# Kernel tuning notes

Measured on AMD Instinct MI355X. Metric: run time of the kernel, lower is better.

The kernel has to match this reference:

```python
import jax, jax.numpy as jnp
import numpy as np

N_NODES = 100000
N_EDGES = 3200000
F_IN = 512
HIDDEN = 64
N_CLASSES = 64


def setup_inputs() -> dict:
    key = jax.random.key(0)
    ks = jax.random.split(key, 6)
    node_features = jax.random.normal(ks[0], (N_NODES, F_IN), dtype=jnp.float32)
    edge_rows = jax.random.randint(ks[1], (N_EDGES,), 0, N_NODES, dtype=jnp.int32)
    edge_cols = jax.random.randint(ks[2], (N_EDGES,), 0, N_NODES, dtype=jnp.int32)
    edge_vals = jax.random.uniform(ks[3], (N_EDGES,), dtype=jnp.float32)
    W1 = jax.random.normal(ks[4], (F_IN, HIDDEN), dtype=jnp.float32) / np.sqrt(F_IN)
    b1 = jnp.zeros((HIDDEN,), dtype=jnp.float32)
    W2 = jax.random.normal(ks[5], (HIDDEN, N_CLASSES), dtype=jnp.float32) / np.sqrt(HIDDEN)
    b2 = jnp.zeros((N_CLASSES,), dtype=jnp.float32)
    return {
        "node_features": node_features,
        "edge_rows": edge_rows,
        "edge_cols": edge_cols,
        "edge_vals": edge_vals,
        "W1": W1,
        "b1": b1,
        "W2": W2,
        "b2": b2,
    }


def reference(node_features, edge_rows, edge_cols, edge_vals, W1, b1, W2, b2):
    # MLP node transform (inference: dropout is identity, no norms)
    h = jax.nn.relu(node_features @ W1 + b1)          # [N, HIDDEN]
    logits = h @ W2 + b2                              # [N, C]
    # smoother @ logits : sparse [N,N] COO times dense [N,C]
    messages = edge_vals[:, None] * logits[edge_cols]  # [E, C]
    out = jax.ops.segment_sum(messages, edge_rows, num_segments=N_NODES)
    return out
```

## Files before the change

kernel.cpp:

```cpp
#include <hip/hip_runtime.h>
#include <hip/hip_bf16.h>
#include <stdint.h>

#define N_NODES 100000
#define N_EDGES 3200000
#define F_IN    512
#define HIDDEN  64
#define NCLS    64

#define BROWS   128
#define NBKT    782
#define NBKT_PAD 1024
#define CHUNK   4096
#define EPB     16384
#define NCB     ((N_EDGES + EPB - 1) / EPB)

typedef float v4f __attribute__((ext_vector_type(4)));
typedef short v8s __attribute__((ext_vector_type(8)));

__device__ __forceinline__ unsigned short f2bf(float f){
  unsigned u = __float_as_uint(f);
  u += 0x7fffu + ((u >> 16) & 1u);
  return (unsigned short)(u >> 16);
}
__device__ __forceinline__ float bflo(unsigned u){ return __uint_as_float(u << 16); }
__device__ __forceinline__ float bfhi(unsigned u){ return __uint_as_float(u & 0xffff0000u); }

__global__ void prep_weights(const float* __restrict__ W1, const float* __restrict__ W2,
                             unsigned short* __restrict__ w1f, unsigned short* __restrict__ w2f){
  int t = blockIdx.x * 256 + threadIdx.x;
  if (t < 16*4*64*8){
    int j = t & 7, lane = (t >> 3) & 63, nt = (t >> 9) & 3, ks = t >> 11;
    int m = lane & 15, q = lane >> 4;
    int k = ks*32 + q*8 + j, n = nt*16 + m;
    w1f[t] = f2bf(W1[k*HIDDEN + n]);
  } else {
    int u = t - 16*4*64*8;
    if (u < 2*4*64*8){
      int j = u & 7, lane = (u >> 3) & 63, nt = (u >> 9) & 3, ks = u >> 11;
      int m = lane & 15, q = lane >> 4;
      int k = ks*32 + q*8 + j, n = nt*16 + m;
      w2f[u] = f2bf(W2[k*NCLS + n]);
    }
  }
}

__global__ __launch_bounds__(256) void mlp_kernel(
    const float* __restrict__ X, const float* __restrict__ b1,
    const float* __restrict__ b2,
    const unsigned short* __restrict__ w1f, const unsigned short* __restrict__ w2f,
    unsigned short* __restrict__ logits){
  __shared__ __align__(16) float lds[4][16][68];
  int tid  = threadIdx.x;
  int wid  = tid >> 6, lane = tid & 63;
  int m    = lane & 15, q = lane >> 4;
  int base = blockIdx.x * 64 + wid * 16;
  if (base > N_NODES - 16) base = N_NODES - 16;

  const float* rp = X + (size_t)(base + m) * F_IN + q * 8;
  const v8s* w1v = (const v8s*)w1f;
  const v8s* w2v = (const v8s*)w2f;

  v4f a0c = {0,0,0,0}, a1c = {0,0,0,0}, a2c = {0,0,0,0}, a3c = {0,0,0,0};
  #pragma unroll
  for (int ks = 0; ks < 16; ++ks){
    const float4* pa = (const float4*)(rp + ks * 32);
    float4 x0 = pa[0], x1 = pa[1];
    v8s af;
    af[0]=(short)f2bf(x0.x); af[1]=(short)f2bf(x0.y); af[2]=(short)f2bf(x0.z); af[3]=(short)f2bf(x0.w);
    af[4]=(short)f2bf(x1.x); af[5]=(short)f2bf(x1.y); af[6]=(short)f2bf(x1.z); af[7]=(short)f2bf(x1.w);
    a0c = __builtin_amdgcn_mfma_f32_16x16x32_bf16(af, w1v[(ks*4+0)*64 + lane], a0c, 0,0,0);
    a1c = __builtin_amdgcn_mfma_f32_16x16x32_bf16(af, w1v[(ks*4+1)*64 + lane], a1c, 0,0,0);
    a2c = __builtin_amdgcn_mfma_f32_16x16x32_bf16(af, w1v[(ks*4+2)*64 + lane], a2c, 0,0,0);
    a3c = __builtin_amdgcn_mfma_f32_16x16x32_bf16(af, w1v[(ks*4+3)*64 + lane], a3c, 0,0,0);
  }

  float b1v0 = b1[m], b1v1 = b1[16+m], b1v2 = b1[32+m], b1v3 = b1[48+m];
  #pragma unroll
  for (int r = 0; r < 4; ++r){
    int row = q*4 + r;
    lds[wid][row][     m] = fmaxf(a0c[r] + b1v0, 0.f);
    lds[wid][row][16 + m] = fmaxf(a1c[r] + b1v1, 0.f);
    lds[wid][row][32 + m] = fmaxf(a2c[r] + b1v2, 0.f);
    lds[wid][row][48 + m] = fmaxf(a3c[r] + b1v3, 0.f);
  }
  __syncthreads();

  v4f c0 = {0,0,0,0}, c1 = {0,0,0,0}, c2 = {0,0,0,0}, c3 = {0,0,0,0};
  #pragma unroll
  for (int k2 = 0; k2 < 2; ++k2){
    const float4* ph = (const float4*)&lds[wid][m][k2*32 + q*8];
    float4 h0 = ph[0], h1 = ph[1];
    v8s af;
    af[0]=(short)f2bf(h0.x); af[1]=(short)f2bf(h0.y); af[2]=(short)f2bf(h0.z); af[3]=(short)f2bf(h0.w);
    af[4]=(short)f2bf(h1.x); af[5]=(short)f2bf(h1.y); af[6]=(short)f2bf(h1.z); af[7]=(short)f2bf(h1.w);
    c0 = __builtin_amdgcn_mfma_f32_16x16x32_bf16(af, w2v[(k2*4+0)*64 + lane], c0, 0,0,0);
    c1 = __builtin_amdgcn_mfma_f32_16x16x32_bf16(af, w2v[(k2*4+1)*64 + lane], c1, 0,0,0);
    c2 = __builtin_amdgcn_mfma_f32_16x16x32_bf16(af, w2v[(k2*4+2)*64 + lane], c2, 0,0,0);
    c3 = __builtin_amdgcn_mfma_f32_16x16x32_bf16(af, w2v[(k2*4+3)*64 + lane], c3, 0,0,0);
  }

  float b2v0 = b2[m], b2v1 = b2[16+m], b2v2 = b2[32+m], b2v3 = b2[48+m];
  unsigned short* lp = logits + (size_t)base * NCLS;
  #pragma unroll
  for (int r = 0; r < 4; ++r){
    int row = q*4 + r;
    lp[row*NCLS +      m] = f2bf(c0[r] + b2v0);
    lp[row*NCLS + 16 + m] = f2bf(c1[r] + b2v1);
    lp[row*NCLS + 32 + m] = f2bf(c2[r] + b2v2);
    lp[row*NCLS + 48 + m] = f2bf(c3[r] + b2v3);
  }
}

__global__ __launch_bounds__(256) void bucket_count(
    const int* __restrict__ rows, int* __restrict__ bcnt){
  __shared__ int lc[NBKT_PAD];
  int t = threadIdx.x;
  #pragma unroll
  for (int i = 0; i < 4; ++i) lc[t*4 + i] = 0;
  __syncthreads();
  int base = blockIdx.x * EPB;
  int cnt  = min(EPB, N_EDGES - base);
  const int4* rp = (const int4*)(rows + base);
  int nv = cnt >> 2;
  for (int i = t; i < nv; i += 256){
    int4 r = rp[i];
    atomicAdd(&lc[r.x >> 7], 1);
    atomicAdd(&lc[r.y >> 7], 1);
    atomicAdd(&lc[r.z >> 7], 1);
    atomicAdd(&lc[r.w >> 7], 1);
  }
  __syncthreads();
  for (int i = t; i < NBKT; i += 256){
    int v = lc[i];
    if (v) atomicAdd(&bcnt[i], v);
  }
}

__global__ __launch_bounds__(256) void bucket_scan(
    const int* __restrict__ bcnt, int* __restrict__ bbase, int* __restrict__ bcur,
    int* __restrict__ offs){
  __shared__ int ssum[256];
  int t = threadIdx.x;
  int v[4]; int s = 0;
  #pragma unroll
  for (int k = 0; k < 4; ++k){
    int i = t*4 + k;
    v[k] = (i < NBKT) ? bcnt[i] : 0;
    s += v[k];
  }
  ssum[t] = s; __syncthreads();
  for (int o = 1; o < 256; o <<= 1){
    int add = (t >= o) ? ssum[t - o] : 0;
    __syncthreads();
    ssum[t] += add;
    __syncthreads();
  }
  int run = ssum[t] - s;
  #pragma unroll
  for (int k = 0; k < 4; ++k){
    int i = t*4 + k;
    if (i < NBKT){ bbase[i] = run; bcur[i] = run; run += v[k]; }
  }
  if (t == 0){ bbase[NBKT] = N_EDGES; offs[N_NODES] = N_EDGES; }
}

__global__ __launch_bounds__(256) void bucket_scatter(
    const int* __restrict__ rows, const int* __restrict__ cols,
    const float* __restrict__ vals, int* __restrict__ bcur,
    int2* __restrict__ ebkt){
  __shared__ int  lcnt[NBKT_PAD];
  __shared__ int  lbase[NBKT_PAD];
  __shared__ int  ssum[256];
  __shared__ int2 stage[CHUNK];
  __shared__ int  sdst[CHUNK];
  int t = threadIdx.x;
  int base = blockIdx.x * CHUNK;
  int cnt  = min(CHUNK, N_EDGES - base);

  #pragma unroll
  for (int i = 0; i < 4; ++i) lcnt[t*4 + i] = 0;
  __syncthreads();

  int r[16];
  #pragma unroll
  for (int k = 0; k < 16; ++k){
    int li = t + k*256;
    if (li < cnt){
      r[k] = rows[base + li];
      atomicAdd(&lcnt[r[k] >> 7], 1);
    } else r[k] = -1;
  }
  __syncthreads();

  int v0 = lcnt[t*4], v1 = lcnt[t*4+1], v2 = lcnt[t*4+2], v3 = lcnt[t*4+3];
  int s = v0 + v1 + v2 + v3;
  ssum[t] = s; __syncthreads();
  for (int o = 1; o < 256; o <<= 1){
    int add = (t >= o) ? ssum[t - o] : 0;
    __syncthreads();
    ssum[t] += add;
    __syncthreads();
  }
  int run = ssum[t] - s;
  int e0 = run, e1 = run + v0, e2 = run + v0 + v1, e3 = run + v0 + v1 + v2;
  if (v0){ int g = atomicAdd(&bcur[t*4+0], v0); lbase[t*4+0] = g - e0; }
  if (v1){ int g = atomicAdd(&bcur[t*4+1], v1); lbase[t*4+1] = g - e1; }
  if (v2){ int g = atomicAdd(&bcur[t*4+2], v2); lbase[t*4+2] = g - e2; }
  if (v3){ int g = atomicAdd(&bcur[t*4+3], v3); lbase[t*4+3] = g - e3; }
  lcnt[t*4+0] = e0; lcnt[t*4+1] = e1; lcnt[t*4+2] = e2; lcnt[t*4+3] = e3;
  __syncthreads();

  #pragma unroll
  for (int k = 0; k < 16; ++k){
    if (r[k] >= 0){
      int li = t + k*256;
      int c  = cols[base + li];
      float v = vals[base + li];
      int b  = r[k] >> 7;
      int pos = atomicAdd(&lcnt[b], 1);
      stage[pos] = make_int2(((r[k] & 127) << 17) | c, __float_as_int(v));
      sdst[pos]  = lbase[b];
    }
  }
  __syncthreads();

  for (int j = t; j < cnt; j += 256){
    ebkt[sdst[j] + j] = stage[j];
  }
}

__global__ __launch_bounds__(256) void bucket_sort(
    const int* __restrict__ bbase, const int2* __restrict__ ebkt,
    int2* __restrict__ edges, int* __restrict__ offs){
  __shared__ int rc[BROWS];
  __shared__ int sc[BROWS];
  __shared__ int cur[BROWS];
  int b = blockIdx.x, t = threadIdx.x;
  int row0 = b * BROWS;
  int s = bbase[b], e = bbase[b + 1];
  if (t < BROWS) rc[t] = 0;
  __syncthreads();
  for (int i = s + t; i < e; i += 256){
    int lr = ((unsigned)ebkt[i].x) >> 17;
    atomicAdd(&rc[lr], 1);
  }
  __syncthreads();
  if (t < BROWS) sc[t] = rc[t];
  __syncthreads();
  for (int o = 1; o < BROWS; o <<= 1){
    int add = (t >= o && t < BROWS) ? sc[t - o] : 0;
    __syncthreads();
    if (t < BROWS) sc[t] += add;
    __syncthreads();
  }
  if (t < BROWS){
    int off0 = s + sc[t] - rc[t];
    cur[t] = off0;
    int rr = row0 + t;
    if (rr < N_NODES) offs[rr] = off0;
  }
  __syncthreads();
  for (int i = s + t; i < e; i += 256){
    int2 ev = ebkt[i];
    int lr  = ((unsigned)ev.x) >> 17;
    int pos = atomicAdd(&cur[lr], 1);
    edges[pos] = make_int2(ev.x & 0x1FFFF, ev.y);
  }
}

__global__ __launch_bounds__(256) void agg_kernel(
    const int* __restrict__ offs, const int2* __restrict__ edges,
    const unsigned short* __restrict__ logits, float* __restrict__ out){
  int n    = blockIdx.x * 4 + (threadIdx.x >> 6);
  int lane = threadIdx.x & 63;
  int h    = lane & 15;
  int sel  = lane >> 4;
  int s = offs[n], e = offs[n + 1];
  const uint2* lg = (const uint2*)logits;

  float a0 = 0.f, a1 = 0.f, a2 = 0.f, a3 = 0.f;
  int i = s;
  for (; i + 16 <= e; i += 16){
    int2 e0 = edges[i      + sel];
    int2 e1 = edges[i + 4  + sel];
    int2 e2 = edges[i + 8  + sel];
    int2 e3 = edges[i + 12 + sel];
    uint2 u0 = lg[((size_t)e0.x << 4) + h];
    uint2 u1 = lg[((size_t)e1.x << 4) + h];
    uint2 u2 = lg[((size_t)e2.x << 4) + h];
    uint2 u3 = lg[((size_t)e3.x << 4) + h];
    float v0 = __int_as_float(e0.y), v1 = __int_as_float(e1.y);
    float v2 = __int_as_float(e2.y), v3 = __int_as_float(e3.y);
    a0 = fmaf(v0, bflo(u0.x), a0); a1 = fmaf(v0, bfhi(u0.x), a1);
    a2 = fmaf(v0, bflo(u0.y), a2); a3 = fmaf(v0, bfhi(u0.y), a3);
    a0 = fmaf(v1, bflo(u1.x), a0); a1 = fmaf(v1, bfhi(u1.x), a1);
    a2 = fmaf(v1, bflo(u1.y), a2); a3 = fmaf(v1, bfhi(u1.y), a3);
    a0 = fmaf(v2, bflo(u2.x), a0); a1 = fmaf(v2, bfhi(u2.x), a1);
    a2 = fmaf(v2, bflo(u2.y), a2); a3 = fmaf(v2, bfhi(u2.y), a3);
    a0 = fmaf(v3, bflo(u3.x), a0); a1 = fmaf(v3, bfhi(u3.x), a1);
    a2 = fmaf(v3, bflo(u3.y), a2); a3 = fmaf(v3, bfhi(u3.y), a3);
  }
  for (; i < e; i += 4){
    int idx = i + sel;
    int col = 0; float v = 0.f;
    if (idx < e){ int2 ev = edges[idx]; col = ev.x; v = __int_as_float(ev.y); }
    uint2 u = lg[((size_t)col << 4) + h];
    a0 = fmaf(v, bflo(u.x), a0); a1 = fmaf(v, bfhi(u.x), a1);
    a2 = fmaf(v, bflo(u.y), a2); a3 = fmaf(v, bfhi(u.y), a3);
  }
  a0 += __shfl_xor(a0, 16); a0 += __shfl_xor(a0, 32);
  a1 += __shfl_xor(a1, 16); a1 += __shfl_xor(a1, 32);
  a2 += __shfl_xor(a2, 16); a2 += __shfl_xor(a2, 32);
  a3 += __shfl_xor(a3, 16); a3 += __shfl_xor(a3, 32);
  if (sel == 0){
    float4* op = (float4*)(out + (size_t)n * NCLS);
    op[h] = make_float4(a0, a1, a2, a3);
  }
}

__global__ void scatter_atomic(const int* __restrict__ rows, const int* __restrict__ cols,
                               const float* __restrict__ vals,
                               const unsigned short* __restrict__ logits,
                               float* __restrict__ out){
  long g = (long)blockIdx.x * 256 + threadIdx.x;
  int e = (int)(g >> 6), c = (int)(g & 63);
  if (e < N_EDGES){
    float lv = __uint_as_float(((unsigned)logits[(size_t)cols[e] * NCLS + c]) << 16);
    atomicAdd(&out[(size_t)rows[e] * NCLS + c], vals[e] * lv);
  }
}

extern "C" void kernel_launch(void* const* d_in, const int* in_sizes, int n_in,
                              void* d_out, int out_size, void* d_ws, size_t ws_size,
                              hipStream_t stream){
  const float* X     = (const float*)d_in[0];
  const int*   erows = (const int*)  d_in[1];
  const int*   ecols = (const int*)  d_in[2];
  const float* evals = (const float*)d_in[3];
  const float* W1    = (const float*)d_in[4];
  const float* b1    = (const float*)d_in[5];
  const float* W2    = (const float*)d_in[6];
  const float* b2    = (const float*)d_in[7];
  float* out = (float*)d_out;

  char* ws = (char*)d_ws;
  size_t off = 0;
  auto alloc = [&](size_t bytes) -> char* {
    char* p = ws + off;
    off = (off + bytes + 255) & ~(size_t)255;
    return p;
  };
  unsigned short* logits = (unsigned short*)alloc((size_t)N_NODES * NCLS * 2);
  unsigned short* w1f    = (unsigned short*)alloc(16*4*64*8 * 2);
  unsigned short* w2f    = (unsigned short*)alloc(2*4*64*8 * 2);
  int* offs  = (int*)alloc((size_t)(N_NODES + 1) * 4);
  int* bcnt  = (int*)alloc((size_t)NBKT * 4);
  int* bbase = (int*)alloc((size_t)(NBKT + 1) * 4);
  int* bcur  = (int*)alloc((size_t)NBKT * 4);
  int2* ebkt  = (int2*)alloc((size_t)N_EDGES * 8);
  int2* edges = (int2*)alloc((size_t)N_EDGES * 8);
  size_t full_need = off;

  prep_weights<<<144, 256, 0, stream>>>(W1, W2, w1f, w2f);
  mlp_kernel<<<(N_NODES + 63) / 64, 256, 0, stream>>>(X, b1, b2, w1f, w2f, logits);

  if (ws_size >= full_need){
    hipMemsetAsync(bcnt, 0, (size_t)NBKT * 4, stream);
    bucket_count  <<<NCB, 256, 0, stream>>>(erows, bcnt);
    bucket_scan   <<<1, 256, 0, stream>>>(bcnt, bbase, bcur, offs);
    bucket_scatter<<<(N_EDGES + CHUNK - 1) / CHUNK, 256, 0, stream>>>(erows, ecols, evals, bcur, ebkt);
    bucket_sort   <<<NBKT, 256, 0, stream>>>(bbase, ebkt, edges, offs);
    agg_kernel    <<<N_NODES / 4, 256, 0, stream>>>(offs, edges, logits, out);
  } else {
    hipMemsetAsync(out, 0, (size_t)N_NODES * NCLS * 4, stream);
    scatter_atomic<<<(int)(((long)N_EDGES * 64 + 255) / 256), 256, 0, stream>>>(
        erows, ecols, evals, logits, out);
  }
}
```

Measured before the change: 519.4 us.

## Replace count/scan/sort pipeline with fixed-capacity buckets and LDS atomic aggregation

Drops the bucket count, scan and per-row sort kernels. Edges are now scattered into fixed-capacity per-bucket slots (CAP entries each), with a small overflow list, and a new per-bucket kernel accumulates 128 rows x 64 classes in shared memory using LDS atomics. Overflow edges are applied afterwards with global atomics, and counter zeroing is folded into the weight-prep kernel. This removes several launches and a full pass over the edge data, at the cost of heavy LDS atomic traffic and a capacity limit that leans on the roughly uniform row distribution.

```diff
diff --git a/kernel.cpp b/kernel.cpp
--- a/kernel.cpp
+++ b/kernel.cpp
@@ -12,8 +12,9 @@
 #define NBKT    782
 #define NBKT_PAD 1024
 #define CHUNK   4096
-#define EPB     16384
-#define NCB     ((N_EDGES + EPB - 1) / EPB)
+#define CAP     4608
+#define OVF_CAP 8192
+#define SENTINEL ((int)0x80000000)
 
 typedef float v4f __attribute__((ext_vector_type(4)));
 typedef short v8s __attribute__((ext_vector_type(8)));
@@ -24,11 +25,12 @@
   return (unsigned short)(u >> 16);
 }
 __device__ __forceinline__ float bflo(unsigned u){ return __uint_as_float(u << 16); }
-__device__ __forceinline__ float bfhi(unsigned u){ return __uint_as_float(u & 0xffff0000u); }
 
 __global__ void prep_weights(const float* __restrict__ W1, const float* __restrict__ W2,
-                             unsigned short* __restrict__ w1f, unsigned short* __restrict__ w2f){
+                             unsigned short* __restrict__ w1f, unsigned short* __restrict__ w2f,
+                             int* __restrict__ zeroc){
   int t = blockIdx.x * 256 + threadIdx.x;
+  if (t < NBKT*16 + 16) zeroc[t] = 0;
   if (t < 16*4*64*8){
     int j = t & 7, lane = (t >> 3) & 63, nt = (t >> 9) & 3, ks = t >> 11;
     int m = lane & 15, q = lane >> 4;
@@ -112,62 +114,10 @@
   }
 }
 
-__global__ __launch_bounds__(256) void bucket_count(
-    const int* __restrict__ rows, int* __restrict__ bcnt){
-  __shared__ int lc[NBKT_PAD];
-  int t = threadIdx.x;
-  #pragma unroll
-  for (int i = 0; i < 4; ++i) lc[t*4 + i] = 0;
-  __syncthreads();
-  int base = blockIdx.x * EPB;
-  int cnt  = min(EPB, N_EDGES - base);
-  const int4* rp = (const int4*)(rows + base);
-  int nv = cnt >> 2;
-  for (int i = t; i < nv; i += 256){
-    int4 r = rp[i];
-    atomicAdd(&lc[r.x >> 7], 1);
-    atomicAdd(&lc[r.y >> 7], 1);
-    atomicAdd(&lc[r.z >> 7], 1);
-    atomicAdd(&lc[r.w >> 7], 1);
-  }
-  __syncthreads();
-  for (int i = t; i < NBKT; i += 256){
-    int v = lc[i];
-    if (v) atomicAdd(&bcnt[i], v);
-  }
-}
-
-__global__ __launch_bounds__(256) void bucket_scan(
-    const int* __restrict__ bcnt, int* __restrict__ bbase, int* __restrict__ bcur,
-    int* __restrict__ offs){
-  __shared__ int ssum[256];
-  int t = threadIdx.x;
-  int v[4]; int s = 0;
-  #pragma unroll
-  for (int k = 0; k < 4; ++k){
-    int i = t*4 + k;
-    v[k] = (i < NBKT) ? bcnt[i] : 0;
-    s += v[k];
-  }
-  ssum[t] = s; __syncthreads();
-  for (int o = 1; o < 256; o <<= 1){
-    int add = (t >= o) ? ssum[t - o] : 0;
-    __syncthreads();
-    ssum[t] += add;
-    __syncthreads();
-  }
-  int run = ssum[t] - s;
-  #pragma unroll
-  for (int k = 0; k < 4; ++k){
-    int i = t*4 + k;
-    if (i < NBKT){ bbase[i] = run; bcur[i] = run; run += v[k]; }
-  }
-  if (t == 0){ bbase[NBKT] = N_EDGES; offs[N_NODES] = N_EDGES; }
-}
-
 __global__ __launch_bounds__(256) void bucket_scatter(
     const int* __restrict__ rows, const int* __restrict__ cols,
     const float* __restrict__ vals, int* __restrict__ bcur,
+    int* __restrict__ ovf_cnt, int4* __restrict__ ovf,
     int2* __restrict__ ebkt){
   __shared__ int  lcnt[NBKT_PAD];
   __shared__ int  lbase[NBKT_PAD];
@@ -204,10 +154,10 @@
   }
   int run = ssum[t] - s;
   int e0 = run, e1 = run + v0, e2 = run + v0 + v1, e3 = run + v0 + v1 + v2;
-  if (v0){ int g = atomicAdd(&bcur[t*4+0], v0); lbase[t*4+0] = g - e0; }
-  if (v1){ int g = atomicAdd(&bcur[t*4+1], v1); lbase[t*4+1] = g - e1; }
-  if (v2){ int g = atomicAdd(&bcur[t*4+2], v2); lbase[t*4+2] = g - e2; }
-  if (v3){ int g = atomicAdd(&bcur[t*4+3], v3); lbase[t*4+3] = g - e3; }
+  if (v0){ int g = atomicAdd(&bcur[(t*4+0)*16], v0); lbase[t*4+0] = (t*4+0)*CAP + g - e0; }
+  if (v1){ int g = atomicAdd(&bcur[(t*4+1)*16], v1); lbase[t*4+1] = (t*4+1)*CAP + g - e1; }
+  if (v2){ int g = atomicAdd(&bcur[(t*4+2)*16], v2); lbase[t*4+2] = (t*4+2)*CAP + g - e2; }
+  if (v3){ int g = atomicAdd(&bcur[(t*4+3)*16], v3); lbase[t*4+3] = (t*4+3)*CAP + g - e3; }
   lcnt[t*4+0] = e0; lcnt[t*4+1] = e1; lcnt[t*4+2] = e2; lcnt[t*4+3] = e3;
   __syncthreads();
 
@@ -219,103 +169,81 @@
       float v = vals[base + li];
       int b  = r[k] >> 7;
       int pos = atomicAdd(&lcnt[b], 1);
-      stage[pos] = make_int2(((r[k] & 127) << 17) | c, __float_as_int(v));
-      sdst[pos]  = lbase[b];
+      int dest = lbase[b] + pos;
+      if (dest < b*CAP + CAP){
+        stage[pos] = make_int2(((r[k] & 127) << 17) | c, __float_as_int(v));
+        sdst[pos]  = lbase[b];
+      } else {
+        sdst[pos] = SENTINEL;
+        int o = atomicAdd(ovf_cnt, 1);
+        if (o < OVF_CAP) ovf[o] = make_int4(r[k], c, __float_as_int(v), 0);
+      }
     }
   }
   __syncthreads();
 
   for (int j = t; j < cnt; j += 256){
-    ebkt[sdst[j] + j] = stage[j];
-  }
-}
-
-__global__ __launch_bounds__(256) void bucket_sort(
-    const int* __restrict__ bbase, const int2* __restrict__ ebkt,
-    int2* __restrict__ edges, int* __restrict__ offs){
-  __shared__ int rc[BROWS];
-  __shared__ int sc[BROWS];
-  __shared__ int cur[BROWS];
+    int d = sdst[j];
+    if (d != SENTINEL) ebkt[d + j] = stage[j];
+  }
+}
+
+__global__ __launch_bounds__(256) void bucket_agg(
+    const int* __restrict__ bcur, const int2* __restrict__ ebkt,
+    const unsigned short* __restrict__ logits, float* __restrict__ out){
+  __shared__ float acc[BROWS * 64];
   int b = blockIdx.x, t = threadIdx.x;
+  int w = t >> 6, lane = t & 63;
+
+  float4* accv = (float4*)acc;
+  for (int j = t; j < BROWS * 16; j += 256) accv[j] = make_float4(0.f, 0.f, 0.f, 0.f);
+  __syncthreads();
+
+  int cnt = bcur[b * 16];
+  if (cnt > CAP) cnt = CAP;
+  const int2* ep = ebkt + (size_t)b * CAP;
+
+  #define UNR 8
+  for (int i0 = w * UNR; i0 < cnt; i0 += 4 * UNR){
+    int2 ev[UNR];
+    #pragma unroll
+    for (int k = 0; k < UNR; ++k)
+      ev[k] = (i0 + k < cnt) ? ep[i0 + k] : make_int2(0, 0);
+    float pv[UNR]; int srow[UNR];
+    #pragma unroll
+    for (int k = 0; k < UNR; ++k){
+      int x  = __builtin_amdgcn_readfirstlane(ev[k].x);
+      int vb = __builtin_amdgcn_readfirstlane(ev[k].y);
+      unsigned short u = logits[((size_t)(x & 0x1FFFF) << 6) + lane];
+      pv[k]   = __int_as_float(vb) * bflo(u);
+      srow[k] = (int)(((unsigned)x >> 17) << 6);
+    }
+    #pragma unroll
+    for (int k = 0; k < UNR; ++k)
+      atomicAdd(&acc[srow[k] + lane], pv[k]);
+  }
+  #undef UNR
+  __syncthreads();
+
   int row0 = b * BROWS;
-  int s = bbase[b], e = bbase[b + 1];
-  if (t < BROWS) rc[t] = 0;
-  __syncthreads();
-  for (int i = s + t; i < e; i += 256){
-    int lr = ((unsigned)ebkt[i].x) >> 17;
-    atomicAdd(&rc[lr], 1);
-  }
-  __syncthreads();
-  if (t < BROWS) sc[t] = rc[t];
-  __syncthreads();
-  for (int o = 1; o < BROWS; o <<= 1){
-    int add = (t >= o && t < BROWS) ? sc[t - o] : 0;
-    __syncthreads();
-    if (t < BROWS) sc[t] += add;
-    __syncthreads();
-  }
-  if (t < BROWS){
-    int off0 = s + sc[t] - rc[t];
-    cur[t] = off0;
-    int rr = row0 + t;
-    if (rr < N_NODES) offs[rr] = off0;
-  }
-  __syncthreads();
-  for (int i = s + t; i < e; i += 256){
-    int2 ev = ebkt[i];
-    int lr  = ((unsigned)ev.x) >> 17;
-    int pos = atomicAdd(&cur[lr], 1);
-    edges[pos] = make_int2(ev.x & 0x1FFFF, ev.y);
-  }
-}
-
-__global__ __launch_bounds__(256) void agg_kernel(
-    const int* __restrict__ offs, const int2* __restrict__ edges,
+  for (int j = t; j < BROWS * 16; j += 256){
+    int row = j >> 4;
+    if (row0 + row < N_NODES)
+      ((float4*)(out + ((size_t)(row0 + row) << 6)))[j & 15] = accv[j];
+  }
+}
+
+__global__ __launch_bounds__(256) void ovf_apply(
+    const int* __restrict__ ovf_cnt, const int4* __restrict__ ovf,
     const unsigned short* __restrict__ logits, float* __restrict__ out){
-  int n    = blockIdx.x * 4 + (threadIdx.x >> 6);
-  int lane = threadIdx.x & 63;
-  int h    = lane & 15;
-  int sel  = lane >> 4;
-  int s = offs[n], e = offs[n + 1];
-  const uint2* lg = (const uint2*)logits;
-
-  float a0 = 0.f, a1 = 0.f, a2 = 0.f, a3 = 0.f;
-  int i = s;
-  for (; i + 16 <= e; i += 16){
-    int2 e0 = edges[i      + sel];
-    int2 e1 = edges[i + 4  + sel];
-    int2 e2 = edges[i + 8  + sel];
-    int2 e3 = edges[i + 12 + sel];
-    uint2 u0 = lg[((size_t)e0.x << 4) + h];
-    uint2 u1 = lg[((size_t)e1.x << 4) + h];
-    uint2 u2 = lg[((size_t)e2.x << 4) + h];
-    uint2 u3 = lg[((size_t)e3.x << 4) + h];
-    float v0 = __int_as_float(e0.y), v1 = __int_as_float(e1.y);
-    float v2 = __int_as_float(e2.y), v3 = __int_as_float(e3.y);
-    a0 = fmaf(v0, bflo(u0.x), a0); a1 = fmaf(v0, bfhi(u0.x), a1);
-    a2 = fmaf(v0, bflo(u0.y), a2); a3 = fmaf(v0, bfhi(u0.y), a3);
-    a0 = fmaf(v1, bflo(u1.x), a0); a1 = fmaf(v1, bfhi(u1.x), a1);
-    a2 = fmaf(v1, bflo(u1.y), a2); a3 = fmaf(v1, bfhi(u1.y), a3);
-    a0 = fmaf(v2, bflo(u2.x), a0); a1 = fmaf(v2, bfhi(u2.x), a1);
-    a2 = fmaf(v2, bflo(u2.y), a2); a3 = fmaf(v2, bfhi(u2.y), a3);
-    a0 = fmaf(v3, bflo(u3.x), a0); a1 = fmaf(v3, bfhi(u3.x), a1);
-    a2 = fmaf(v3, bflo(u3.y), a2); a3 = fmaf(v3, bfhi(u3.y), a3);
-  }
-  for (; i < e; i += 4){
-    int idx = i + sel;
-    int col = 0; float v = 0.f;
-    if (idx < e){ int2 ev = edges[idx]; col = ev.x; v = __int_as_float(ev.y); }
-    uint2 u = lg[((size_t)col << 4) + h];
-    a0 = fmaf(v, bflo(u.x), a0); a1 = fmaf(v, bfhi(u.x), a1);
-    a2 = fmaf(v, bflo(u.y), a2); a3 = fmaf(v, bfhi(u.y), a3);
-  }
-  a0 += __shfl_xor(a0, 16); a0 += __shfl_xor(a0, 32);
-  a1 += __shfl_xor(a1, 16); a1 += __shfl_xor(a1, 32);
-  a2 += __shfl_xor(a2, 16); a2 += __shfl_xor(a2, 32);
-  a3 += __shfl_xor(a3, 16); a3 += __shfl_xor(a3, 32);
-  if (sel == 0){
-    float4* op = (float4*)(out + (size_t)n * NCLS);
-    op[h] = make_float4(a0, a1, a2, a3);
+  int cnt = ovf_cnt[0];
+  if (cnt > OVF_CAP) cnt = OVF_CAP;
+  long total = (long)cnt * 64;
+  for (long i = (long)blockIdx.x * 256 + threadIdx.x; i < total; i += (long)gridDim.x * 256){
+    int e = (int)(i >> 6), c = (int)(i & 63);
+    int4 ev = ovf[e];
+    float lv = bflo(logits[((size_t)ev.y << 6) + c]);
+    atomicAdd(&out[((size_t)ev.x << 6) + c], __int_as_float(ev.z) * lv);
   }
 }
 
@@ -354,24 +282,20 @@
   unsigned short* logits = (unsigned short*)alloc((size_t)N_NODES * NCLS * 2);
   unsigned short* w1f    = (unsigned short*)alloc(16*4*64*8 * 2);
   unsigned short* w2f    = (unsigned short*)alloc(2*4*64*8 * 2);
-  int* offs  = (int*)alloc((size_t)(N_NODES + 1) * 4);
-  int* bcnt  = (int*)alloc((size_t)NBKT * 4);
-  int* bbase = (int*)alloc((size_t)(NBKT + 1) * 4);
-  int* bcur  = (int*)alloc((size_t)NBKT * 4);
-  int2* ebkt  = (int2*)alloc((size_t)N_EDGES * 8);
-  int2* edges = (int2*)alloc((size_t)N_EDGES * 8);
+  int*  bcur = (int*)alloc((size_t)(NBKT*16 + 16) * 4);
+  int*  ovfc = bcur + NBKT*16;
+  int4* ovf  = (int4*)alloc((size_t)OVF_CAP * 16);
+  int2* ebkt = (int2*)alloc((size_t)NBKT * CAP * 8);
   size_t full_need = off;
 
-  prep_weights<<<144, 256, 0, stream>>>(W1, W2, w1f, w2f);
+  prep_weights<<<144, 256, 0, stream>>>(W1, W2, w1f, w2f, bcur);
   mlp_kernel<<<(N_NODES + 63) / 64, 256, 0, stream>>>(X, b1, b2, w1f, w2f, logits);
 
   if (ws_size >= full_need){
-    hipMemsetAsync(bcnt, 0, (size_t)NBKT * 4, stream);
-    bucket_count  <<<NCB, 256, 0, stream>>>(erows, bcnt);
-    bucket_scan   <<<1, 256, 0, stream>>>(bcnt, bbase, bcur, offs);
-    bucket_scatter<<<(N_EDGES + CHUNK - 1) / CHUNK, 256, 0, stream>>>(erows, ecols, evals, bcur, ebkt);
-    bucket_sort   <<<NBKT, 256, 0, stream>>>(bbase, ebkt, edges, offs);
-    agg_kernel    <<<N_NODES / 4, 256, 0, stream>>>(offs, edges, logits, out);
+    bucket_scatter<<<(N_EDGES + CHUNK - 1) / CHUNK, 256, 0, stream>>>(
+        erows, ecols, evals, bcur, ovfc, ovf, ebkt);
+    bucket_agg<<<NBKT, 256, 0, stream>>>(bcur, ebkt, logits, out);
+    ovf_apply<<<256, 256, 0, stream>>>(ovfc, ovf, logits, out);
   } else {
     hipMemsetAsync(out, 0, (size_t)N_NODES * NCLS * 4, stream);
     scatter_atomic<<<(int)(((long)N_EDGES * 64 + 255) / 256), 256, 0, stream>>>(
```

Result: slower. 1.735 ms (+234.0%).
